# Optimization experiments

Hardware: AMD Instinct MI355X
Metric: run time of the kernel (lower is better)

## Reference

```python
import jax, jax.numpy as jnp
import numpy as np

BN_EPS = 1e-5
# regular 3x3 kernel grid offsets: row0 = dy, row1 = dx, kernel positions in row-major order
REG = jnp.array([[-1, -1, -1, 0, 0, 0, 1, 1, 1],
                 [-1,  0,  1, -1, 0, 1, -1, 0, 1]], dtype=jnp.float32)


def conv3x3(x, w, b):
    y = jax.lax.conv_general_dilated(x, w, window_strides=(1, 1),
                                     padding=((1, 1), (1, 1)),
                                     dimension_numbers=('NCHW', 'OIHW', 'NCHW'))
    return y + b[None, :, None, None]


def deform_conv3x3(x, dy, dx, w):
    # x: [N,C,H,W]; dy,dx: [N,9,H,W] per-kernel-tap offsets; w: [O,C,3,3]
    N, C, H, W = x.shape
    K = 9
    ky = jnp.repeat(jnp.arange(3), 3)   # [0,0,0,1,1,1,2,2,2]
    kx = jnp.tile(jnp.arange(3), 3)     # [0,1,2,0,1,2,0,1,2]
    # sampling positions: p = p_out - pad + k*dilation + offset (stride=1, pad=dil=1)
    py = dy + (jnp.arange(H) - 1)[None, None, :, None] + ky[None, :, None, None].astype(x.dtype)
    px = dx + (jnp.arange(W) - 1)[None, None, None, :] + kx[None, :, None, None].astype(x.dtype)
    y0 = jnp.floor(py)
    x0 = jnp.floor(px)
    wy = py - y0  # bilinear weights
    wx = px - x0
    y0i = y0.astype(jnp.int32)
    x0i = x0.astype(jnp.int32)
    nidx = jnp.arange(N)[:, None, None, None]

    def gather(yi, xi):
        valid = ((yi >= 0) & (yi < H) & (xi >= 0) & (xi < W)).astype(x.dtype)
        v = x[nidx, :, jnp.clip(yi, 0, H - 1), jnp.clip(xi, 0, W - 1)]  # [N,K,H,W,C]
        return v * valid[..., None]

    sampled = (gather(y0i,     x0i)     * ((1 - wy) * (1 - wx))[..., None]
             + gather(y0i,     x0i + 1) * ((1 - wy) * wx)[..., None]
             + gather(y0i + 1, x0i)     * (wy * (1 - wx))[..., None]
             + gather(y0i + 1, x0i + 1) * (wy * wx)[..., None])  # [N,K,H,W,C]
    O = w.shape[0]
    return jnp.einsum('nkhwc,ock->nohw', sampled, w.reshape(O, C, K))


def setup_inputs() -> dict:
    key = jax.random.key(0)
    ks = jax.random.split(key, 12)
    N, C, H, W = 2, 256, 96, 96
    O = 256
    sc = 1.0 / np.sqrt(C * 9)
    return {
        'x': jax.random.normal(ks[0], (N, C, H, W), jnp.float32),
        'mask_attention': jax.random.normal(ks[1], (N, C, H, W), jnp.float32),
        'w_tm': jax.random.normal(ks[2], (4, C, 3, 3), jnp.float32) * sc,
        'b_tm': jax.random.normal(ks[3], (4,), jnp.float32) * 0.01,
        'w_tr': jax.random.normal(ks[4], (2, C, 3, 3), jnp.float32) * sc,
        'b_tr': jax.random.normal(ks[5], (2,), jnp.float32) * 0.01,
        'w_deform': jax.random.normal(ks[6], (O, C, 3, 3), jnp.float32) * sc,
        'bn_gamma': jnp.ones((O,), jnp.float32),
        'bn_beta': jnp.zeros((O,), jnp.float32),
        'bn_mean': jax.random.normal(ks[7], (O,), jnp.float32) * 0.01,
        'bn_var': jax.random.uniform(ks[8], (O,), jnp.float32, 0.5, 1.5),
    }


def reference(x, mask_attention, w_tm, b_tm, w_tr, b_tr, w_deform,
              bn_gamma, bn_beta, bn_mean, bn_var):
    # mask_attention is overwritten by x in the original forward; ignored.
    N, C, H, W = x.shape
    tm = conv3x3(x, w_tm, b_tm)                       # [N,4,H,W]
    T = tm.transpose(0, 2, 3, 1).reshape(N, H, W, 2, 2)
    off = jnp.einsum('nhwij,jk->nhwik', T, REG) - REG  # [N,H,W,2,9], (T-I)@REG
    tr = conv3x3(x, w_tr, b_tr)                        # [N,2,H,W]
    off = off + tr.transpose(0, 2, 3, 1)[..., None]    # broadcast translation to all 9 taps
    dy = off[..., 0, :].transpose(0, 3, 1, 2)          # [N,9,H,W]
    dx = off[..., 1, :].transpose(0, 3, 1, 2)
    out = deform_conv3x3(x, dy, dx, w_deform)          # [N,O,H,W]
    inv = jax.lax.rsqrt(bn_var + BN_EPS)
    out = (out - bn_mean[None, :, None, None]) * (inv * bn_gamma)[None, :, None, None] \
          + bn_beta[None, :, None, None]
    return jax.nn.relu(out + x)
```

## Files before the change

### kernel.cpp

```cpp
#include <hip/hip_runtime.h>
#include <stdint.h>

#define H_ 96
#define W_ 96
#define C_ 256
#define O_ 256
#define N_ 2
#define HW_ (H_*W_)
#define M_ (N_*HW_)
#define GK 2304

typedef _Float16 f16x8 __attribute__((ext_vector_type(8)));
typedef _Float16 f16x2 __attribute__((ext_vector_type(2)));
typedef float f32x4 __attribute__((ext_vector_type(4)));
typedef unsigned short us4 __attribute__((ext_vector_type(4)));
typedef unsigned short us8 __attribute__((ext_vector_type(8)));

__device__ __forceinline__ unsigned short f2h(float f) {
  union { _Float16 h; unsigned short u; } v;
  v.h = (_Float16)f;
  return v.u;
}
__device__ __forceinline__ f16x2 hpair(float f) {
  const _Float16 h = (_Float16)f;
  return (f16x2){h, h};
}

__global__ __launch_bounds__(256) void k_pre(const float* __restrict__ x,
                                             const float* __restrict__ w_df,
                                             const float* __restrict__ w_tm,
                                             const float* __restrict__ w_tr,
                                             unsigned short* __restrict__ xt,
                                             unsigned short* __restrict__ wfrag,
                                             unsigned short* __restrict__ w6p) {
  const int b = blockIdx.x;
  const int tid = threadIdx.x;
  if (b < 576) {
    __shared__ unsigned short tile[64][130];
    const int pt = b % 144;
    const int ch = (b / 144) & 1;
    const int n  = b / 288;
    const int p0 = pt * 64, c0 = ch * 128;
    const float* xp = x + (size_t)n * C_ * HW_;
    unsigned short* xtp = xt + (size_t)n * C_ * HW_;
    const int tx = tid & 15, ty = tid >> 4;
#pragma unroll
    for (int pass = 0; pass < 8; pass++) {
      const int c = pass * 16 + ty;
      const f32x4 v = *(const f32x4*)(xp + (size_t)(c0 + c) * HW_ + p0 + tx * 4);
#pragma unroll
      for (int i = 0; i < 4; i++) tile[tx * 4 + i][c] = f2h(v[i]);
    }
    __syncthreads();
    const int l32 = tid & 31, pr = tid >> 5;
#pragma unroll
    for (int pass = 0; pass < 8; pass++) {
      const int p = pass * 8 + pr;
      us4 v;
#pragma unroll
      for (int i = 0; i < 4; i++) v[i] = tile[p][l32 * 4 + i];
      *(us4*)(xtp + (size_t)(p0 + p) * C_ + c0 + l32 * 4) = v;
    }
  } else if (b < 864) {
    const int base = (b - 576) * 2048 + tid * 8;
    const int l  = (base >> 3) & 63;
    const int g  = (base >> 9) & 15;
    const int ks = (base >> 13) & 7;
    const int t  = base >> 16;
    const int o  = g * 16 + (l & 15);
    const int c  = ks * 32 + (l >> 4) * 8;
    us8 res;
#pragma unroll
    for (int j = 0; j < 8; j++) res[j] = f2h(w_df[(size_t)(o * 256 + c + j) * 9 + t]);
    *(us8*)(wfrag + base) = res;
  } else {
    int idx = (b - 864) * 256 + tid;
    int t = idx >> 12;
    int r = idx & 4095;
    int j = r >> 8;
    int c = r & 255;
    float v = 0.f;
    if (j < 4) v = w_tm[(size_t)(j * C_ + c) * 9 + t];
    else if (j < 6) v = w_tr[(size_t)((j - 4) * C_ + c) * 9 + t];
    w6p[idx] = f2h(v);
  }
}

__global__ __launch_bounds__(512, 2) void k_fused(const unsigned short* __restrict__ xt,
                                                  const unsigned short* __restrict__ Wfrag,
                                                  const unsigned short* __restrict__ w6p,
                                                  const float* __restrict__ b_tm,
                                                  const float* __restrict__ b_tr,
                                                  const float* __restrict__ xres,
                                                  const float* __restrict__ gamma,
                                                  const float* __restrict__ beta,
                                                  const float* __restrict__ mean,
                                                  const float* __restrict__ var,
                                                  float* __restrict__ out) {
  __shared__ unsigned short As[2][2][32 * 256] __attribute__((aligned(16)));
  __shared__ float sred[8][16][8];
  __shared__ float coords_s[2][32][9][2];
  const int tid = threadIdx.x;
  const int wave = tid >> 6, lane = tid & 63;
  const int row = lane & 15, quad = lane >> 4;
  const int bm = (blockIdx.x & 7) * 36 + (blockIdx.x >> 3);
  const int m0 = bm * 32;
  const int sr = tid >> 4;
  const int cg = tid & 15;

  for (int s = 0; s < 2; ++s) {
    const unsigned short* xts = xt + (size_t)s * C_ * HW_;
    {
      const int h = m0 / W_;
      const int w0 = m0 - h * W_;
      const int rh = wave >> 2;
      const int cq = (wave & 3) * 64;
      f32x4 oacc = {0.f, 0.f, 0.f, 0.f};
      const f16x8 zero8 = {};
#pragma unroll
      for (int t = 0; t < 9; t++) {
        const int ty = t / 3, tx = t % 3;
        const int y = h + ty - 1;
        if (y < 0 || y >= H_) continue;
        const int xx = w0 + rh * 16 + row + tx - 1;
        const bool valid = (xx >= 0) && (xx < W_);
        const int xc = min(max(xx, 0), W_ - 1);
        const unsigned short* arow = xts + (size_t)(y * W_ + xc) * C_ + cq + quad * 8;
        const unsigned short* brow = w6p + (size_t)(t * 16 + row) * C_ + cq + quad * 8;
#pragma unroll
        for (int ks = 0; ks < 2; ks++) {
          f16x8 av = *(const f16x8*)(const void*)(arow + ks * 32);
          if (!valid) av = zero8;
          f16x8 bv = *(const f16x8*)(const void*)(brow + ks * 32);
          oacc = __builtin_amdgcn_mfma_f32_16x16x32_f16(av, bv, oacc, 0, 0, 0);
        }
      }
      if (row < 6) {
#pragma unroll
        for (int r = 0; r < 4; r++) sred[wave][quad * 4 + r][row] = oacc[r];
      }
    }
    __syncthreads();
    if (wave < 2 && lane < 16) {
      const int rg = wave * 16 + lane;
      const int hwm = m0 + rg;
      const int h = hwm / W_, w = hwm - h * W_;
      float a[6];
#pragma unroll
      for (int j = 0; j < 6; j++)
        a[j] = sred[wave * 4 + 0][lane][j] + sred[wave * 4 + 1][lane][j] +
               sred[wave * 4 + 2][lane][j] + sred[wave * 4 + 3][lane][j];
      const float tm0 = a[0] + b_tm[0];
      const float tm1 = a[1] + b_tm[1];
      const float tm2 = a[2] + b_tm[2];
      const float tm3 = a[3] + b_tm[3];
      const float tr0 = a[4] + b_tr[0];
      const float tr1 = a[5] + b_tr[1];
#pragma unroll
      for (int t = 0; t < 9; t++) {
        const float ry = (float)(t / 3) - 1.f;
        const float rx = (float)(t % 3) - 1.f;
        coords_s[s][rg][t][0] = (float)h + tr0 + tm0 * ry + tm1 * rx;
        coords_s[s][rg][t][1] = (float)w + tr1 + tm2 * ry + tm3 * rx;
      }
    }
    __syncthreads();
  }

  f32x4 acc[2][2][2] = {};
  f16x2 cwh0, cwh1, cwh2, cwh3;
  int cb[4];
  us8 u0[4], u1[4];

#define PREP1(TAP, S)                                                          \
  {                                                                            \
    const float py = coords_s[S][sr][TAP][0];                                  \
    const float px = coords_s[S][sr][TAP][1];                                  \
    const float fy = floorf(py), fx = floorf(px);                              \
    const float wy = py - fy, wx = px - fx;                                    \
    const int y0 = (int)fy, x0 = (int)fx;                                      \
    const int y1 = y0 + 1, x1 = x0 + 1;                                        \
    const float vy0 = (y0 >= 0 && y0 < H_) ? 1.f : 0.f;                        \
    const float vy1 = (y1 >= 0 && y1 < H_) ? 1.f : 0.f;                        \
    const float vx0 = (x0 >= 0 && x0 < W_) ? 1.f : 0.f;                        \
    const float vx1 = (x1 >= 0 && x1 < W_) ? 1.f : 0.f;                        \
    cwh0 = hpair((1.f - wy) * (1.f - wx) * vy0 * vx0);                         \
    cwh1 = hpair((1.f - wy) * wx * vy0 * vx1);                                 \
    cwh2 = hpair(wy * (1.f - wx) * vy1 * vx0);                                 \
    cwh3 = hpair(wy * wx * vy1 * vx1);                                         \
    const int cy0 = min(max(y0, 0), H_ - 1), cy1 = min(max(y1, 0), H_ - 1);    \
    const int cx0 = min(max(x0, 0), W_ - 1), cx1 = min(max(x1, 0), W_ - 1);    \
    cb[0] = (cy0 * W_ + cx0) * C_;                                             \
    cb[1] = (cy0 * W_ + cx1) * C_;                                             \
    cb[2] = (cy1 * W_ + cx0) * C_;                                             \
    cb[3] = (cy1 * W_ + cx1) * C_;                                             \
  }

#define LOADC1(XB)                                                             \
  {                                                                            \
    const int cc = cg * 16;                                                    \
    u0[0] = *(const us8*)(XB + cb[0] + cc); u1[0] = *(const us8*)(XB + cb[0] + cc + 8); \
    u0[1] = *(const us8*)(XB + cb[1] + cc); u1[1] = *(const us8*)(XB + cb[1] + cc + 8); \
    u0[2] = *(const us8*)(XB + cb[2] + cc); u1[2] = *(const us8*)(XB + cb[2] + cc + 8); \
    u0[3] = *(const us8*)(XB + cb[3] + cc); u1[3] = *(const us8*)(XB + cb[3] + cc + 8); \
  }

#define LERP8V(DST, U)                                                         \
  {                                                                            \
    const f16x2* p0 = (const f16x2*)&U[0];                                     \
    const f16x2* p1 = (const f16x2*)&U[1];                                     \
    const f16x2* p2 = (const f16x2*)&U[2];                                     \
    const f16x2* p3 = (const f16x2*)&U[3];                                     \
    f16x2* d = (f16x2*)&DST;                                                   \
    _Pragma("unroll")                                                          \
    for (int p = 0; p < 4; p++) {                                              \
      f16x2 r = p0[p] * cwh0;                                                  \
      r = p1[p] * cwh1 + r;                                                    \
      r = p2[p] * cwh2 + r;                                                    \
      r = p3[p] * cwh3 + r;                                                    \
      d[p] = r;                                                                \
    }                                                                          \
  }

#define STAGE(TAP, S, XB)                                                      \
  {                                                                            \
    PREP1(TAP, S);                                                             \
    LOADC1(XB);                                                                \
    unsigned short* asb = &As[(TAP) & 1][S][0];                                \
    const int q0i = cg * 2, q1i = cg * 2 + 1;                                  \
    const int s0 = (q0i & 24) | ((q0i ^ sr) & 7);                              \
    const int s1 = (q1i & 24) | ((q1i ^ sr) & 7);                              \
    us8 r0, r1;                                                                \
    LERP8V(r0, u0);                                                            \
    LERP8V(r1, u1);                                                            \
    *(us8*)(void*)&asb[sr * 256 + s0 * 8] = r0;                                \
    *(us8*)(void*)&asb[sr * 256 + s1 * 8] = r1;                                \
  }

  const unsigned short* xt1 = xt + (size_t)C_ * HW_;

  for (int tap = 0; tap < 9; tap++) {
    STAGE(tap, 0, xt);
    STAGE(tap, 1, xt1);

    const unsigned short* wfTap =
        Wfrag + (size_t)tap * 65536 + wave * 1024 + lane * 8;
    f16x8 bv[2];
#pragma unroll
    for (int ot = 0; ot < 2; ot++) bv[ot] = *(const f16x8*)(const void*)(wfTap + ot * 512);
    __builtin_amdgcn_sched_barrier(0);

    __syncthreads();

    const unsigned short* A0 = &As[tap & 1][0][0];
    const unsigned short* A1 = &As[tap & 1][1][0];
#pragma unroll
    for (int ks = 0; ks < 8; ks++) {
      const int q = ks * 4 + quad;
      const int slot = (q & 24) | ((q ^ row) & 7);
      const f16x8 a00 = *(const f16x8*)(const void*)&A0[row * 256 + slot * 8];
      const f16x8 a01 = *(const f16x8*)(const void*)&A0[(row + 16) * 256 + slot * 8];
      const f16x8 a10 = *(const f16x8*)(const void*)&A1[row * 256 + slot * 8];
      const f16x8 a11 = *(const f16x8*)(const void*)&A1[(row + 16) * 256 + slot * 8];
      f16x8 bn[2];
      if (ks < 7) {
        const unsigned short* wfn = wfTap + (size_t)(ks + 1) * 8192;
#pragma unroll
        for (int ot = 0; ot < 2; ot++) bn[ot] = *(const f16x8*)(const void*)(wfn + ot * 512);
      }
#pragma unroll
      for (int ot = 0; ot < 2; ot++) {
        acc[0][0][ot] = __builtin_amdgcn_mfma_f32_16x16x32_f16(a00, bv[ot], acc[0][0][ot], 0, 0, 0);
        acc[0][1][ot] = __builtin_amdgcn_mfma_f32_16x16x32_f16(a01, bv[ot], acc[0][1][ot], 0, 0, 0);
        acc[1][0][ot] = __builtin_amdgcn_mfma_f32_16x16x32_f16(a10, bv[ot], acc[1][0][ot], 0, 0, 0);
        acc[1][1][ot] = __builtin_amdgcn_mfma_f32_16x16x32_f16(a11, bv[ot], acc[1][1][ot], 0, 0, 0);
      }
      if (ks < 7) {
#pragma unroll
        for (int ot = 0; ot < 2; ot++) bv[ot] = bn[ot];
      }
    }
  }

  const int hwb = m0 + quad * 4;
#pragma unroll
  for (int ot = 0; ot < 2; ot++) {
    const int o = wave * 32 + ot * 16 + row;
    const float sc = rsqrtf(var[o] + 1e-5f) * gamma[o];
    const float bi = beta[o] - mean[o] * sc;
#pragma unroll
    for (int s = 0; s < 2; ++s) {
      const size_t ob0 = (size_t)(s * O_ + o) * HW_ + hwb;
      f32x4 rv = *(const f32x4*)(xres + ob0);
      f32x4 ov;
#pragma unroll
      for (int r = 0; r < 4; r++) ov[r] = fmaxf(acc[s][0][ot][r] * sc + bi + rv[r], 0.f);
      *(f32x4*)(out + ob0) = ov;
      const size_t ob1 = ob0 + 16;
      rv = *(const f32x4*)(xres + ob1);
#pragma unroll
      for (int r = 0; r < 4; r++) ov[r] = fmaxf(acc[s][1][ot][r] * sc + bi + rv[r], 0.f);
      *(f32x4*)(out + ob1) = ov;
    }
  }
}

extern "C" void kernel_launch(void* const* d_in, const int* in_sizes, int n_in,
                              void* d_out, int out_size, void* d_ws, size_t ws_size,
                              hipStream_t stream) {
  const float* x     = (const float*)d_in[0];
  const float* w_tm  = (const float*)d_in[2];
  const float* b_tm  = (const float*)d_in[3];
  const float* w_tr  = (const float*)d_in[4];
  const float* b_tr  = (const float*)d_in[5];
  const float* w_df  = (const float*)d_in[6];
  const float* gamma = (const float*)d_in[7];
  const float* beta  = (const float*)d_in[8];
  const float* mean  = (const float*)d_in[9];
  const float* var   = (const float*)d_in[10];
  float* out = (float*)d_out;

  char* ws = (char*)d_ws;
  unsigned short* xt    = (unsigned short*)(ws);
  unsigned short* wfrag = (unsigned short*)(ws + 9437184);
  unsigned short* w6p   = (unsigned short*)(ws + 9437184 + 1179648);

  k_pre<<<1008, 256, 0, stream>>>(x, w_df, w_tm, w_tr, xt, wfrag, w6p);
  k_fused<<<288, 512, 0, stream>>>(xt, wfrag, w6p, b_tm, b_tr, x,
                                   gamma, beta, mean, var, out);
}
```

Baseline: 184.5 us.

## Rebalance work to 256 blocks with 80- or 64-row flattened M tiles

Replaces the 288-block grid, where each block handled 32 pixels for both batch images, with 256 blocks covering flattened batch-spatial rows. 128 blocks take 80 rows and 128 take 64. This aims to match the grid to the CU count, avoiding a partial second wave, and to raise weight (B fragment) reuse per block. The offset-conv prologue is also restructured into 16-row tiles with an 8-wave reduction. The cost is a larger LDS footprint (80x256 A buffers, double-buffered), more registers for five accumulator tiles, and load imbalance between the 80-row and 64-row blocks.

```diff
diff --git a/kernel.cpp b/kernel.cpp
--- a/kernel.cpp
+++ b/kernel.cpp
@@ -97,24 +97,29 @@
                                                   const float* __restrict__ mean,
                                                   const float* __restrict__ var,
                                                   float* __restrict__ out) {
-  __shared__ unsigned short As[2][2][32 * 256] __attribute__((aligned(16)));
-  __shared__ float sred[8][16][8];
-  __shared__ float coords_s[2][32][9][2];
+  __shared__ unsigned short As[2][80 * 256] __attribute__((aligned(16)));
+  __shared__ float sred5[5][8][16][8];
+  __shared__ float coords_s[80][9][2];
+  __shared__ int   nofs[80];
   const int tid = threadIdx.x;
   const int wave = tid >> 6, lane = tid & 63;
   const int row = lane & 15, quad = lane >> 4;
-  const int bm = (blockIdx.x & 7) * 36 + (blockIdx.x >> 3);
-  const int m0 = bm * 32;
+  const int pb = (blockIdx.x & 7) * 32 + (blockIdx.x >> 3);
+  const bool fat = pb < 128;
+  const int nt = fat ? 5 : 4;
+  const int m0 = fat ? pb * 80 : 10240 + (pb - 128) * 64;
   const int sr = tid >> 4;
   const int cg = tid & 15;
 
-  for (int s = 0; s < 2; ++s) {
-    const unsigned short* xts = xt + (size_t)s * C_ * HW_;
-    {
-      const int h = m0 / W_;
-      const int w0 = m0 - h * W_;
-      const int rh = wave >> 2;
-      const int cq = (wave & 3) * 64;
+#pragma unroll
+  for (int t5 = 0; t5 < 5; ++t5) {
+    if (t5 < nt) {
+      const int ts = m0 + t5 * 16;
+      const int nn = ts / HW_;
+      const int hw = ts - nn * HW_;
+      const int h = hw / W_, w0 = hw - h * W_;
+      const unsigned short* xts = xt + (size_t)nn * C_ * HW_;
+      const int cq = wave * 32;
       f32x4 oacc = {0.f, 0.f, 0.f, 0.f};
       const f16x8 zero8 = {};
 #pragma unroll
@@ -122,60 +127,64 @@
         const int ty = t / 3, tx = t % 3;
         const int y = h + ty - 1;
         if (y < 0 || y >= H_) continue;
-        const int xx = w0 + rh * 16 + row + tx - 1;
+        const int xx = w0 + row + tx - 1;
         const bool valid = (xx >= 0) && (xx < W_);
         const int xc = min(max(xx, 0), W_ - 1);
-        const unsigned short* arow = xts + (size_t)(y * W_ + xc) * C_ + cq + quad * 8;
-        const unsigned short* brow = w6p + (size_t)(t * 16 + row) * C_ + cq + quad * 8;
-#pragma unroll
-        for (int ks = 0; ks < 2; ks++) {
-          f16x8 av = *(const f16x8*)(const void*)(arow + ks * 32);
-          if (!valid) av = zero8;
-          f16x8 bv = *(const f16x8*)(const void*)(brow + ks * 32);
-          oacc = __builtin_amdgcn_mfma_f32_16x16x32_f16(av, bv, oacc, 0, 0, 0);
-        }
+        f16x8 av = *(const f16x8*)(const void*)(xts + (size_t)(y * W_ + xc) * C_ + cq + quad * 8);
+        if (!valid) av = zero8;
+        const f16x8 bv = *(const f16x8*)(const void*)(w6p + (size_t)(t * 16 + row) * C_ + cq + quad * 8);
+        oacc = __builtin_amdgcn_mfma_f32_16x16x32_f16(av, bv, oacc, 0, 0, 0);
       }
       if (row < 6) {
 #pragma unroll
-        for (int r = 0; r < 4; r++) sred[wave][quad * 4 + r][row] = oacc[r];
-      }
-    }
-    __syncthreads();
-    if (wave < 2 && lane < 16) {
-      const int rg = wave * 16 + lane;
-      const int hwm = m0 + rg;
-      const int h = hwm / W_, w = hwm - h * W_;
-      float a[6];
-#pragma unroll
-      for (int j = 0; j < 6; j++)
-        a[j] = sred[wave * 4 + 0][lane][j] + sred[wave * 4 + 1][lane][j] +
-               sred[wave * 4 + 2][lane][j] + sred[wave * 4 + 3][lane][j];
-      const float tm0 = a[0] + b_tm[0];
-      const float tm1 = a[1] + b_tm[1];
-      const float tm2 = a[2] + b_tm[2];
-      const float tm3 = a[3] + b_tm[3];
-      const float tr0 = a[4] + b_tr[0];
-      const float tr1 = a[5] + b_tr[1];
-#pragma unroll
-      for (int t = 0; t < 9; t++) {
-        const float ry = (float)(t / 3) - 1.f;
-        const float rx = (float)(t % 3) - 1.f;
-        coords_s[s][rg][t][0] = (float)h + tr0 + tm0 * ry + tm1 * rx;
-        coords_s[s][rg][t][1] = (float)w + tr1 + tm2 * ry + tm3 * rx;
-      }
-    }
-    __syncthreads();
-  }
-
-  f32x4 acc[2][2][2] = {};
+        for (int r = 0; r < 4; r++) sred5[t5][wave][quad * 4 + r][row] = oacc[r];
+      }
+    }
+  }
+  __syncthreads();
+  if (tid < nt * 16) {
+    const int rg = tid;
+    const int gm = m0 + rg;
+    const int nn = gm / HW_;
+    const int hw = gm - nn * HW_;
+    const int h = hw / W_, w = hw - h * W_;
+    const int tt = rg >> 4, mm = rg & 15;
+    float a[6];
+#pragma unroll
+    for (int j = 0; j < 6; j++) {
+      float s = 0.f;
+#pragma unroll
+      for (int wv = 0; wv < 8; wv++) s += sred5[tt][wv][mm][j];
+      a[j] = s;
+    }
+    const float tm0 = a[0] + b_tm[0];
+    const float tm1 = a[1] + b_tm[1];
+    const float tm2 = a[2] + b_tm[2];
+    const float tm3 = a[3] + b_tm[3];
+    const float tr0 = a[4] + b_tr[0];
+    const float tr1 = a[5] + b_tr[1];
+#pragma unroll
+    for (int t = 0; t < 9; t++) {
+      const float ry = (float)(t / 3) - 1.f;
+      const float rx = (float)(t % 3) - 1.f;
+      coords_s[rg][t][0] = (float)h + tr0 + tm0 * ry + tm1 * rx;
+      coords_s[rg][t][1] = (float)w + tr1 + tm2 * ry + tm3 * rx;
+    }
+    nofs[rg] = nn * (C_ * HW_);
+  }
+  __syncthreads();
+
+  f32x4 acc[5][2] = {};
   f16x2 cwh0, cwh1, cwh2, cwh3;
   int cb[4];
   us8 u0[4], u1[4];
 
-#define PREP1(TAP, S)                                                          \
+#define STAGEROW(R, TAP, ASB)                                                  \
   {                                                                            \
-    const float py = coords_s[S][sr][TAP][0];                                  \
-    const float px = coords_s[S][sr][TAP][1];                                  \
+    const int r_ = (R);                                                        \
+    const int nof = nofs[r_];                                                  \
+    const float py = coords_s[r_][TAP][0];                                     \
+    const float px = coords_s[r_][TAP][1];                                     \
     const float fy = floorf(py), fx = floorf(px);                              \
     const float wy = py - fy, wx = px - fx;                                    \
     const int y0 = (int)fy, x0 = (int)fx;                                      \
@@ -190,58 +199,55 @@
     cwh3 = hpair(wy * wx * vy1 * vx1);                                         \
     const int cy0 = min(max(y0, 0), H_ - 1), cy1 = min(max(y1, 0), H_ - 1);    \
     const int cx0 = min(max(x0, 0), W_ - 1), cx1 = min(max(x1, 0), W_ - 1);    \
-    cb[0] = (cy0 * W_ + cx0) * C_;                                             \
-    cb[1] = (cy0 * W_ + cx1) * C_;                                             \
-    cb[2] = (cy1 * W_ + cx0) * C_;                                             \
-    cb[3] = (cy1 * W_ + cx1) * C_;                                             \
-  }
-
-#define LOADC1(XB)                                                             \
-  {                                                                            \
+    cb[0] = nof + (cy0 * W_ + cx0) * C_;                                       \
+    cb[1] = nof + (cy0 * W_ + cx1) * C_;                                       \
+    cb[2] = nof + (cy1 * W_ + cx0) * C_;                                       \
+    cb[3] = nof + (cy1 * W_ + cx1) * C_;                                       \
     const int cc = cg * 16;                                                    \
-    u0[0] = *(const us8*)(XB + cb[0] + cc); u1[0] = *(const us8*)(XB + cb[0] + cc + 8); \
-    u0[1] = *(const us8*)(XB + cb[1] + cc); u1[1] = *(const us8*)(XB + cb[1] + cc + 8); \
-    u0[2] = *(const us8*)(XB + cb[2] + cc); u1[2] = *(const us8*)(XB + cb[2] + cc + 8); \
-    u0[3] = *(const us8*)(XB + cb[3] + cc); u1[3] = *(const us8*)(XB + cb[3] + cc + 8); \
-  }
-
-#define LERP8V(DST, U)                                                         \
-  {                                                                            \
-    const f16x2* p0 = (const f16x2*)&U[0];                                     \
-    const f16x2* p1 = (const f16x2*)&U[1];                                     \
-    const f16x2* p2 = (const f16x2*)&U[2];                                     \
-    const f16x2* p3 = (const f16x2*)&U[3];                                     \
-    f16x2* d = (f16x2*)&DST;                                                   \
-    _Pragma("unroll")                                                          \
-    for (int p = 0; p < 4; p++) {                                              \
-      f16x2 r = p0[p] * cwh0;                                                  \
-      r = p1[p] * cwh1 + r;                                                    \
-      r = p2[p] * cwh2 + r;                                                    \
-      r = p3[p] * cwh3 + r;                                                    \
-      d[p] = r;                                                                \
+    u0[0] = *(const us8*)(xt + cb[0] + cc); u1[0] = *(const us8*)(xt + cb[0] + cc + 8); \
+    u0[1] = *(const us8*)(xt + cb[1] + cc); u1[1] = *(const us8*)(xt + cb[1] + cc + 8); \
+    u0[2] = *(const us8*)(xt + cb[2] + cc); u1[2] = *(const us8*)(xt + cb[2] + cc + 8); \
+    u0[3] = *(const us8*)(xt + cb[3] + cc); u1[3] = *(const us8*)(xt + cb[3] + cc + 8); \
+    us8 r0v, r1v;                                                              \
+    {                                                                          \
+      const f16x2* p0 = (const f16x2*)&u0[0];                                  \
+      const f16x2* p1 = (const f16x2*)&u0[1];                                  \
+      const f16x2* p2 = (const f16x2*)&u0[2];                                  \
+      const f16x2* p3 = (const f16x2*)&u0[3];                                  \
+      f16x2* d = (f16x2*)&r0v;                                                 \
+      _Pragma("unroll")                                                        \
+      for (int p = 0; p < 4; p++) {                                            \
+        f16x2 r = p0[p] * cwh0; r = p1[p] * cwh1 + r;                          \
+        r = p2[p] * cwh2 + r;   r = p3[p] * cwh3 + r;  d[p] = r;               \
+      }                                                                        \
     }                                                                          \
-  }
-
-#define STAGE(TAP, S, XB)                                                      \
-  {                                                                            \
-    PREP1(TAP, S);                                                             \
-    LOADC1(XB);                                                                \
-    unsigned short* asb = &As[(TAP) & 1][S][0];                                \
+    {                                                                          \
+      const f16x2* p0 = (const f16x2*)&u1[0];                                  \
+      const f16x2* p1 = (const f16x2*)&u1[1];                                  \
+      const f16x2* p2 = (const f16x2*)&u1[2];                                  \
+      const f16x2* p3 = (const f16x2*)&u1[3];                                  \
+      f16x2* d = (f16x2*)&r1v;                                                 \
+      _Pragma("unroll")                                                        \
+      for (int p = 0; p < 4; p++) {                                            \
+        f16x2 r = p0[p] * cwh0; r = p1[p] * cwh1 + r;                          \
+        r = p2[p] * cwh2 + r;   r = p3[p] * cwh3 + r;  d[p] = r;               \
+      }                                                                        \
+    }                                                                          \
     const int q0i = cg * 2, q1i = cg * 2 + 1;                                  \
-    const int s0 = (q0i & 24) | ((q0i ^ sr) & 7);                              \
-    const int s1 = (q1i & 24) | ((q1i ^ sr) & 7);                              \
-    us8 r0, r1;                                                                \
-    LERP8V(r0, u0);                                                            \
-    LERP8V(r1, u1);                                                            \
-    *(us8*)(void*)&asb[sr * 256 + s0 * 8] = r0;                                \
-    *(us8*)(void*)&asb[sr * 256 + s1 * 8] = r1;                                \
-  }
-
-  const unsigned short* xt1 = xt + (size_t)C_ * HW_;
+    const int s0 = (q0i & 24) | ((q0i ^ r_) & 7);                              \
+    const int s1 = (q1i & 24) | ((q1i ^ r_) & 7);                              \
+    *(us8*)(void*)&ASB[r_ * 256 + s0 * 8] = r0v;                               \
+    *(us8*)(void*)&ASB[r_ * 256 + s1 * 8] = r1v;                               \
+  }
 
   for (int tap = 0; tap < 9; tap++) {
-    STAGE(tap, 0, xt);
-    STAGE(tap, 1, xt1);
+    unsigned short* __restrict__ asb = &As[tap & 1][0];
+
+    STAGEROW(sr, tap, asb);
+    STAGEROW(sr + 32, tap, asb);
+    if (fat) {
+      if (sr < 16) STAGEROW(sr + 64, tap, asb);
+    }
 
     const unsigned short* wfTap =
         Wfrag + (size_t)tap * 65536 + wave * 1024 + lane * 8;
@@ -252,16 +258,16 @@
 
     __syncthreads();
 
-    const unsigned short* A0 = &As[tap & 1][0][0];
-    const unsigned short* A1 = &As[tap & 1][1][0];
 #pragma unroll
     for (int ks = 0; ks < 8; ks++) {
       const int q = ks * 4 + quad;
       const int slot = (q & 24) | ((q ^ row) & 7);
-      const f16x8 a00 = *(const f16x8*)(const void*)&A0[row * 256 + slot * 8];
-      const f16x8 a01 = *(const f16x8*)(const void*)&A0[(row + 16) * 256 + slot * 8];
-      const f16x8 a10 = *(const f16x8*)(const void*)&A1[row * 256 + slot * 8];
-      const f16x8 a11 = *(const f16x8*)(const void*)&A1[(row + 16) * 256 + slot * 8];
+      f16x8 a0 = *(const f16x8*)(const void*)&asb[(0 * 16 + row) * 256 + slot * 8];
+      f16x8 a1 = *(const f16x8*)(const void*)&asb[(1 * 16 + row) * 256 + slot * 8];
+      f16x8 a2 = *(const f16x8*)(const void*)&asb[(2 * 16 + row) * 256 + slot * 8];
+      f16x8 a3 = *(const f16x8*)(const void*)&asb[(3 * 16 + row) * 256 + slot * 8];
+      f16x8 a4;
+      if (fat) a4 = *(const f16x8*)(const void*)&asb[(4 * 16 + row) * 256 + slot * 8];
       f16x8 bn[2];
       if (ks < 7) {
         const unsigned short* wfn = wfTap + (size_t)(ks + 1) * 8192;
@@ -270,10 +276,15 @@
       }
 #pragma unroll
       for (int ot = 0; ot < 2; ot++) {
-        acc[0][0][ot] = __builtin_amdgcn_mfma_f32_16x16x32_f16(a00, bv[ot], acc[0][0][ot], 0, 0, 0);
-        acc[0][1][ot] = __builtin_amdgcn_mfma_f32_16x16x32_f16(a01, bv[ot], acc[0][1][ot], 0, 0, 0);
-        acc[1][0][ot] = __builtin_amdgcn_mfma_f32_16x16x32_f16(a10, bv[ot], acc[1][0][ot], 0, 0, 0);
-        acc[1][1][ot] = __builtin_amdgcn_mfma_f32_16x16x32_f16(a11, bv[ot], acc[1][1][ot], 0, 0, 0);
+        acc[0][ot] = __builtin_amdgcn_mfma_f32_16x16x32_f16(a0, bv[ot], acc[0][ot], 0, 0, 0);
+        acc[1][ot] = __builtin_amdgcn_mfma_f32_16x16x32_f16(a1, bv[ot], acc[1][ot], 0, 0, 0);
+        acc[2][ot] = __builtin_amdgcn_mfma_f32_16x16x32_f16(a2, bv[ot], acc[2][ot], 0, 0, 0);
+        acc[3][ot] = __builtin_amdgcn_mfma_f32_16x16x32_f16(a3, bv[ot], acc[3][ot], 0, 0, 0);
+      }
+      if (fat) {
+#pragma unroll
+        for (int ot = 0; ot < 2; ot++)
+          acc[4][ot] = __builtin_amdgcn_mfma_f32_16x16x32_f16(a4, bv[ot], acc[4][ot], 0, 0, 0);
       }
       if (ks < 7) {
 #pragma unroll
@@ -282,25 +293,24 @@
     }
   }
 
-  const int hwb = m0 + quad * 4;
 #pragma unroll
   for (int ot = 0; ot < 2; ot++) {
     const int o = wave * 32 + ot * 16 + row;
     const float sc = rsqrtf(var[o] + 1e-5f) * gamma[o];
     const float bi = beta[o] - mean[o] * sc;
 #pragma unroll
-    for (int s = 0; s < 2; ++s) {
-      const size_t ob0 = (size_t)(s * O_ + o) * HW_ + hwb;
-      f32x4 rv = *(const f32x4*)(xres + ob0);
-      f32x4 ov;
-#pragma unroll
-      for (int r = 0; r < 4; r++) ov[r] = fmaxf(acc[s][0][ot][r] * sc + bi + rv[r], 0.f);
-      *(f32x4*)(out + ob0) = ov;
-      const size_t ob1 = ob0 + 16;
-      rv = *(const f32x4*)(xres + ob1);
-#pragma unroll
-      for (int r = 0; r < 4; r++) ov[r] = fmaxf(acc[s][1][ot][r] * sc + bi + rv[r], 0.f);
-      *(f32x4*)(out + ob1) = ov;
+    for (int t5 = 0; t5 < 5; t5++) {
+      if (t5 < nt) {
+        const int ts = m0 + t5 * 16;
+        const int nn = ts / HW_;
+        const int hw0 = ts - nn * HW_ + quad * 4;
+        const size_t ob = (size_t)(nn * O_ + o) * HW_ + hw0;
+        const f32x4 rv = *(const f32x4*)(xres + ob);
+        f32x4 ov;
+#pragma unroll
+        for (int r = 0; r < 4; r++) ov[r] = fmaxf(acc[t5][ot][r] * sc + bi + rv[r], 0.f);
+        *(f32x4*)(out + ob) = ov;
+      }
     }
   }
 }
@@ -326,6 +336,6 @@
   unsigned short* w6p   = (unsigned short*)(ws + 9437184 + 1179648);
 
   k_pre<<<1008, 256, 0, stream>>>(x, w_df, w_tm, w_tr, xt, wfrag, w6p);
-  k_fused<<<288, 512, 0, stream>>>(xt, wfrag, w6p, b_tm, b_tr, x,
+  k_fused<<<256, 512, 0, stream>>>(xt, wfrag, w6p, b_tm, b_tr, x,
                                    gamma, beta, mean, var, out);
 }
```

After: 162.3 us. 1.14x faster.
